# Optimization experiments

Hardware: AMD Instinct MI355X
Metric: run time of the kernel (lower is better)

The kernel has to match this reference:

```python
import jax, jax.numpy as jnp
import numpy as np

V, E, L, D, B, S = 50000, 512, 1024, 10, 1024, 50
N_NODES = L - 1  # internal Huffman nodes (balanced tree from uniform label counts)
LN_EPS = 1e-5
N_HIDDEN = 10


def _build_tree():
    # balanced binary tree in heap order: node at depth t for leaf l is (2^t - 1) + (l >> (D - t))
    l = np.arange(L)[:, None]
    t = np.arange(D)[None, :]
    bits = ((l >> (D - 1 - t)) & 1).astype(np.int32)          # [L, D] path direction bits
    paths = ((2 ** t - 1) + (l >> (D - t))).astype(np.int32)  # [L, D] internal node ids
    return paths, bits


def setup_inputs() -> dict:
    key = jax.random.key(0)
    k1, k2, k3, k4, k5, k6 = jax.random.split(key, 6)
    paths, bits = _build_tree()
    return {
        "input_ids": jax.random.randint(k1, (B, S), 0, V),
        "emb_table": jax.random.normal(k2, (V, E), dtype=jnp.float32) * 0.02,
        "W_h": jax.random.normal(k3, (E, E), dtype=jnp.float32) * (1.0 / np.sqrt(E)),
        "b_h": jax.random.normal(k4, (E,), dtype=jnp.float32) * 0.01,
        "theta_W": jax.random.normal(k5, (N_NODES, E, 2), dtype=jnp.float32) * (1.0 / np.sqrt(E)),
        "theta_b": jax.random.normal(k6, (N_NODES, 2), dtype=jnp.float32) * 0.01,
        "paths": jnp.asarray(paths),
        "bits": jnp.asarray(bits),
    }


def reference(input_ids, emb_table, W_h, b_h, theta_W, theta_b, paths, bits):
    # embedding + mean pool over sequence
    x = jnp.take(emb_table, input_ids, axis=0).mean(axis=1)  # [B, E]
    # LayerNorm with default (non-learned) affine, created fresh in torch forward
    mu = x.mean(axis=-1, keepdims=True)
    var = x.var(axis=-1, keepdims=True)
    x = (x - mu) * jax.lax.rsqrt(var + LN_EPS)
    # repeated hidden linear (same weights, hidden_num times)
    for _ in range(N_HIDDEN):
        x = x @ W_h + b_h
    # hierarchical softmax: batched 2-way logits at every internal node
    logits = jnp.einsum('be,ned->bnd', x, theta_W) + theta_b  # [B, N, 2]
    probs = jax.nn.softmax(logits, axis=-1)                   # [B, N, 2]
    # gather each class's path probs and multiply along the path
    p = probs[:, paths, bits]                                  # [B, L, D]
    return jnp.prod(p, axis=-1)                                # [B, L]
```

## Files before the change

### kernel.cpp

```cpp
#include <hip/hip_runtime.h>
#include <hip/hip_bf16.h>
#include <math.h>

#define B_  1024
#define S_  50
#define E_  512
#define L_  1024
#define D_  10
#define NN  1023
#define LN_EPS 1e-5f
#define CBLK 72

typedef short short8 __attribute__((ext_vector_type(8)));
typedef float f32x4  __attribute__((ext_vector_type(4)));
typedef unsigned short u16;
typedef unsigned int   u32;

union PackU { unsigned int u[4]; short8 s; };

__device__ inline void split8(const float r[8], short8& hi, short8& lo) {
    PackU H, L;
#pragma unroll
    for (int q = 0; q < 4; ++q) {
        const unsigned int u0 = __float_as_uint(r[2*q+0]);
        const unsigned int u1 = __float_as_uint(r[2*q+1]);
        H.u[q] = (u0 >> 16) | (u1 & 0xFFFF0000u);
        const float h0 = __uint_as_float(u0 & 0xFFFF0000u);
        const float h1 = __uint_as_float(u1 & 0xFFFF0000u);
        const float l0 = r[2*q+0] - h0;
        const float l1 = r[2*q+1] - h1;
        unsigned int p;
        asm("v_cvt_pk_bf16_f32 %0, %1, %2" : "=v"(p) : "v"(l0), "v"(l1));
        L.u[q] = p;
    }
    hi = H.s; lo = L.s;
}

__device__ inline void split1(float v, u16& h, u16& l) {
    const unsigned int u = __float_as_uint(v);
    h = (u16)(u >> 16);
    const float hf = __uint_as_float(u & 0xFFFF0000u);
    const float lo = v - hf;
    unsigned int p;
    asm("v_cvt_pk_bf16_f32 %0, %1, %2" : "=v"(p) : "v"(lo), "v"(lo));
    l = (u16)(p & 0xFFFFu);
}

__device__ inline void split2(float v0, float v1, u32& hw, u32& lw) {
    const unsigned int u0 = __float_as_uint(v0);
    const unsigned int u1 = __float_as_uint(v1);
    hw = (u0 >> 16) | (u1 & 0xFFFF0000u);
    const float h0 = __uint_as_float(u0 & 0xFFFF0000u);
    const float h1 = __uint_as_float(u1 & 0xFFFF0000u);
    const float l0 = v0 - h0;
    const float l1 = v1 - h1;
    asm("v_cvt_pk_bf16_f32 %0, %1, %2" : "=v"(lw) : "v"(l0), "v"(l1));
}

struct BFrag { short8 ah[2], al[2], bh[2], bl[2]; };

__device__ inline void loadB(BFrag& f,
                             const u16* pah0, const u16* pal0,
                             const u16* pah1, const u16* pal1,
                             const u16* pbh0, const u16* pbl0,
                             const u16* pbh1, const u16* pbl1, int off) {
    f.ah[0] = *reinterpret_cast<const short8*>(pah0 + off);
    f.al[0] = *reinterpret_cast<const short8*>(pal0 + off);
    f.ah[1] = *reinterpret_cast<const short8*>(pah1 + off);
    f.al[1] = *reinterpret_cast<const short8*>(pal1 + off);
    f.bh[0] = *reinterpret_cast<const short8*>(pbh0 + off);
    f.bl[0] = *reinterpret_cast<const short8*>(pbl0 + off);
    f.bh[1] = *reinterpret_cast<const short8*>(pbh1 + off);
    f.bl[1] = *reinterpret_cast<const short8*>(pbl1 + off);
}

template<int TERMS>
__device__ inline void compB(const BFrag& f, f32x4 acc[2][2]) {
#pragma unroll
    for (int i = 0; i < 2; ++i)
#pragma unroll
        for (int j = 0; j < 2; ++j) {
            acc[i][j] = __builtin_amdgcn_mfma_f32_16x16x32_bf16(f.ah[i], f.bh[j], acc[i][j], 0, 0, 0);
            acc[i][j] = __builtin_amdgcn_mfma_f32_16x16x32_bf16(f.ah[i], f.bl[j], acc[i][j], 0, 0, 0);
            acc[i][j] = __builtin_amdgcn_mfma_f32_16x16x32_bf16(f.al[i], f.bh[j], acc[i][j], 0, 0, 0);
            if (TERMS == 4)
                acc[i][j] = __builtin_amdgcn_mfma_f32_16x16x32_bf16(f.al[i], f.bl[j], acc[i][j], 0, 0, 0);
        }
}

template<int TERMS>
__device__ inline void gemmB(const u16* pah0, const u16* pal0,
                             const u16* pah1, const u16* pal1,
                             const u16* pbh0, const u16* pbl0,
                             const u16* pbh1, const u16* pbl1,
                             f32x4 acc[2][2]) {
    BFrag f0, f1;
    loadB(f0, pah0, pal0, pah1, pal1, pbh0, pbl0, pbh1, pbl1, 0);
#pragma unroll 1
    for (int kt = 0; kt < 16; kt += 2) {
        loadB(f1, pah0, pal0, pah1, pal1, pbh0, pbl0, pbh1, pbl1, (kt + 1) * 32);
        compB<TERMS>(f0, acc);
        if (kt + 2 < 16) loadB(f0, pah0, pal0, pah1, pal1, pbh0, pbl0, pbh1, pbl1, (kt + 2) * 32);
        compB<TERMS>(f1, acc);
    }
}

__device__ inline void do_embed_row(const int* __restrict__ ids,
                                    const float* __restrict__ emb,
                                    u16* __restrict__ xah, u16* __restrict__ xal, int b) {
    const int t = threadIdx.x;
    float a0 = 0.f, a1 = 0.f;
    const int* idr = ids + b * S_;
#pragma unroll 5
    for (int s = 0; s < S_; ++s) {
        const float2 v = *reinterpret_cast<const float2*>(emb + (long)idr[s] * E_ + 2 * t);
        a0 += v.x;
        a1 += v.y;
    }
    a0 *= (1.f / S_);
    a1 *= (1.f / S_);

    __shared__ float red[256];
    red[t] = a0 + a1;
    __syncthreads();
    for (int off = 128; off > 0; off >>= 1) {
        if (t < off) red[t] += red[t + off];
        __syncthreads();
    }
    const float mean = red[0] * (1.f / E_);
    __syncthreads();
    const float d0 = a0 - mean, d1 = a1 - mean;
    red[t] = d0 * d0 + d1 * d1;
    __syncthreads();
    for (int off = 128; off > 0; off >>= 1) {
        if (t < off) red[t] += red[t + off];
        __syncthreads();
    }
    const float var = red[0] * (1.f / E_);
    const float inv = 1.f / sqrtf(var + LN_EPS);
    u32 hw, lw;
    split2(d0 * inv, d1 * inv, hw, lw);
    *reinterpret_cast<u32*>(xah + (long)b * E_ + 2 * t) = hw;
    *reinterpret_cast<u32*>(xal + (long)b * E_ + 2 * t) = lw;
}

__device__ inline void do_dpack(const float* __restrict__ thW,
                                u16* __restrict__ Dh, u16* __restrict__ Dl, int part) {
    const int total = NN * 256;
    const int nth = 64 * 256;
    for (int p = part * 256 + (int)threadIdx.x; p < total; p += nth) {
        const int n = p >> 8;
        const int kp = p & 255;
        const float4 v = *reinterpret_cast<const float4*>(thW + (long)n * 1024 + kp * 4);
        u32 hw, lw;
        split2(v.y - v.x, v.w - v.z, hw, lw);
        *reinterpret_cast<u32*>(Dh + (long)n * E_ + kp * 2) = hw;
        *reinterpret_cast<u32*>(Dl + (long)n * E_ + kp * 2) = lw;
    }
}

__device__ inline void compose_epilogue(f32x4 acc[2][2], int row_base, int col_base,
                                        int kg, int r_lo,
                                        const float* __restrict__ Bbias,
                                        u16* __restrict__ Ch, u16* __restrict__ Cl,
                                        u16* __restrict__ Th, u16* __restrict__ Tl,
                                        float* __restrict__ cvec) {
#pragma unroll
    for (int j = 0; j < 2; ++j) {
        const int col = col_base + j * 16 + r_lo;
        const float bb = Bbias[col];
#pragma unroll
        for (int i = 0; i < 2; ++i) {
            const int row0 = row_base + i * 16 + kg * 4;
            union { ushort4 v; u16 e[4]; } th, tl;
#pragma unroll
            for (int r2 = 0; r2 < 4; ++r2) {
                const int row = row0 + r2;
                float v = acc[i][j][r2];
                if (row == E_) { v += bb; cvec[col] = v; }
                u16 h, l;
                split1(v, h, l);
                if (row <= E_ && Ch != nullptr) {
                    Ch[(long)row * E_ + col] = h;
                    Cl[(long)row * E_ + col] = l;
                }
                th.e[r2] = h; tl.e[r2] = l;
            }
            if (row0 + 3 < E_) {
                *reinterpret_cast<ushort4*>(Th + (long)col * E_ + row0) = th.v;
                *reinterpret_cast<ushort4*>(Tl + (long)col * E_ + row0) = tl.v;
            }
        }
    }
}

__device__ inline void do_compose0(const float* __restrict__ Wh, const float* __restrict__ bh,
                                   u16* __restrict__ Ch, u16* __restrict__ Cl,
                                   u16* __restrict__ Th, u16* __restrict__ Tl,
                                   float* __restrict__ cvec, int bid) {
    const int tid  = threadIdx.x;
    const int wid  = tid >> 6;
    const int lane = tid & 63;
    const int r_lo = lane & 15;
    const int kg   = lane >> 4;
    const int row_base = (bid >> 3) * 64 + (wid >> 1) * 32;
    const int col_base = (bid & 7) * 64 + (wid & 1) * 32;
    f32x4 acc[2][2] = {};
#pragma unroll 2
    for (int kt = 0; kt < E_; kt += 32) {
        const int ks = kt + kg * 8;
        short8 ah[2], al[2], bhf[2], blf[2];
#pragma unroll
        for (int i = 0; i < 2; ++i) {
            const int row = row_base + i * 16 + r_lo;
            const float* ap = (row < E_) ? (Wh + (long)row * E_ + ks) : (bh + ks);
            const float4 v0 = *reinterpret_cast<const float4*>(ap);
            const float4 v1 = *reinterpret_cast<const float4*>(ap + 4);
            const float rr[8] = {v0.x, v0.y, v0.z, v0.w, v1.x, v1.y, v1.z, v1.w};
            split8(rr, ah[i], al[i]);
        }
#pragma unroll
        for (int j = 0; j < 2; ++j) {
            const int c = col_base + j * 16 + r_lo;
            float rr[8];
#pragma unroll
            for (int q = 0; q < 8; ++q) rr[q] = Wh[(long)(ks + q) * E_ + c];
            split8(rr, bhf[j], blf[j]);
        }
#pragma unroll
        for (int i = 0; i < 2; ++i)
#pragma unroll
            for (int j = 0; j < 2; ++j) {
                acc[i][j] = __builtin_amdgcn_mfma_f32_16x16x32_bf16(ah[i], bhf[j], acc[i][j], 0, 0, 0);
                acc[i][j] = __builtin_amdgcn_mfma_f32_16x16x32_bf16(ah[i], blf[j], acc[i][j], 0, 0, 0);
                acc[i][j] = __builtin_amdgcn_mfma_f32_16x16x32_bf16(al[i], bhf[j], acc[i][j], 0, 0, 0);
                acc[i][j] = __builtin_amdgcn_mfma_f32_16x16x32_bf16(al[i], blf[j], acc[i][j], 0, 0, 0);
            }
    }
    compose_epilogue(acc, row_base, col_base, kg, r_lo, bh, Ch, Cl, Th, Tl, cvec);
}

__device__ inline void do_composeB(const u16* __restrict__ Ah, const u16* __restrict__ Al,
                                   const u16* __restrict__ Bh, const u16* __restrict__ Bl,
                                   const float* __restrict__ Bbias,
                                   u16* __restrict__ Ch, u16* __restrict__ Cl,
                                   u16* __restrict__ Th, u16* __restrict__ Tl,
                                   float* __restrict__ cvec, int bid) {
    const int tid  = threadIdx.x;
    const int wid  = tid >> 6;
    const int lane = tid & 63;
    const int r_lo = lane & 15;
    const int kg   = lane >> 4;
    const int row_base = (bid >> 3) * 64 + (wid >> 1) * 32;
    const int col_base = (bid & 7) * 64 + (wid & 1) * 32;

    int ra0 = row_base + r_lo;        if (ra0 > E_) ra0 = E_;
    int ra1 = row_base + 16 + r_lo;   if (ra1 > E_) ra1 = E_;
    const long rb0 = col_base + r_lo;
    const long rb1 = col_base + 16 + r_lo;

    f32x4 acc[2][2] = {};
    gemmB<4>(Ah + (long)ra0 * E_ + kg * 8, Al + (long)ra0 * E_ + kg * 8,
             Ah + (long)ra1 * E_ + kg * 8, Al + (long)ra1 * E_ + kg * 8,
             Bh + rb0 * E_ + kg * 8,       Bl + rb0 * E_ + kg * 8,
             Bh + rb1 * E_ + kg * 8,       Bl + rb1 * E_ + kg * 8, acc);

    compose_epilogue(acc, row_base, col_base, kg, r_lo, Bbias, Ch, Cl, Th, Tl, cvec);
}

__device__ inline void do_applyB(const u16* __restrict__ Xh, const u16* __restrict__ Xl,
                                 const u16* __restrict__ Mh, const u16* __restrict__ Ml,
                                 const float* __restrict__ cvec,
                                 u16* __restrict__ Yh, u16* __restrict__ Yl,
                                 int tr, int tc) {
    const int tid  = threadIdx.x;
    const int wid  = tid >> 6;
    const int lane = tid & 63;
    const int r_lo = lane & 15;
    const int kg   = lane >> 4;
    const int row_base = tr * 64 + (wid >> 1) * 32;
    const int col_base = tc * 64 + (wid & 1) * 32;

    const long ra0 = row_base + r_lo;
    const long ra1 = row_base + 16 + r_lo;
    const long rb0 = col_base + r_lo;
    const long rb1 = col_base + 16 + r_lo;

    f32x4 acc[2][2] = {};
    gemmB<3>(Xh + ra0 * E_ + kg * 8, Xl + ra0 * E_ + kg * 8,
             Xh + ra1 * E_ + kg * 8, Xl + ra1 * E_ + kg * 8,
             Mh + rb0 * E_ + kg * 8, Ml + rb0 * E_ + kg * 8,
             Mh + rb1 * E_ + kg * 8, Ml + rb1 * E_ + kg * 8, acc);

#pragma unroll
    for (int j = 0; j < 2; ++j) {
        const int col = col_base + j * 16 + r_lo;
        const float bb = cvec[col];
#pragma unroll
        for (int i = 0; i < 2; ++i) {
#pragma unroll
            for (int r2 = 0; r2 < 4; ++r2) {
                const int row = row_base + i * 16 + kg * 4 + r2;
                u16 h, l;
                split1(acc[i][j][r2] + bb, h, l);
                Yh[(long)row * E_ + col] = h;
                Yl[(long)row * E_ + col] = l;
            }
        }
    }
}

__global__ __launch_bounds__(256) void k_fused0(const float* __restrict__ Wh,
                                                const float* __restrict__ bh,
                                                u16* __restrict__ Ch0, u16* __restrict__ Cl0,
                                                u16* __restrict__ Th0, u16* __restrict__ Tl0,
                                                float* __restrict__ cvec0,
                                                const int* __restrict__ ids,
                                                const float* __restrict__ emb,
                                                u16* __restrict__ xah, u16* __restrict__ xal,
                                                const float* __restrict__ thW,
                                                u16* __restrict__ Dh, u16* __restrict__ Dl) {
    const int bid = blockIdx.x;
    if (bid < CBLK)            do_compose0(Wh, bh, Ch0, Cl0, Th0, Tl0, cvec0, bid);
    else if (bid < CBLK + 512) do_embed_row(ids, emb, xah, xal, bid - CBLK);
    else                       do_dpack(thW, Dh, Dl, bid - CBLK - 512);
}

__global__ __launch_bounds__(256) void k_fused1(const u16* __restrict__ Ch0, const u16* __restrict__ Cl0,
                                                const u16* __restrict__ Th0, const u16* __restrict__ Tl0,
                                                const float* __restrict__ cvec0,
                                                u16* __restrict__ Ch1, u16* __restrict__ Cl1,
                                                u16* __restrict__ Th1, u16* __restrict__ Tl1,
                                                float* __restrict__ cvec1,
                                                const int* __restrict__ ids,
                                                const float* __restrict__ emb,
                                                u16* __restrict__ xah, u16* __restrict__ xal) {
    const int bid = blockIdx.x;
    if (bid < CBLK) do_composeB(Ch0, Cl0, Th0, Tl0, cvec0, Ch1, Cl1, Th1, Tl1, cvec1, bid);
    else            do_embed_row(ids, emb, xah, xal, 512 + (bid - CBLK));
}

__global__ __launch_bounds__(256) void k_fused2(const u16* __restrict__ Ch1, const u16* __restrict__ Cl1,
                                                const u16* __restrict__ Th1, const u16* __restrict__ Tl1,
                                                const float* __restrict__ cvec1,
                                                u16* __restrict__ Th2, u16* __restrict__ Tl2,
                                                float* __restrict__ cvec2,
                                                const u16* __restrict__ xah, const u16* __restrict__ xal,
                                                const u16* __restrict__ Th0, const u16* __restrict__ Tl0,
                                                const float* __restrict__ cvec0,
                                                u16* __restrict__ y1h, u16* __restrict__ y1l) {
    const int bid = blockIdx.x;
    if (bid < CBLK) {
        do_composeB(Ch1, Cl1, Th1, Tl1, cvec1, nullptr, nullptr, Th2, Tl2, cvec2, bid);
    } else {
        const int t = bid - CBLK;
        do_applyB(xah, xal, Th0, Tl0, cvec0, y1h, y1l, t >> 3, t & 7);
    }
}

__global__ __launch_bounds__(256) void k_apply8(const u16* __restrict__ y1h, const u16* __restrict__ y1l,
                                                const u16* __restrict__ Th2, const u16* __restrict__ Tl2,
                                                const float* __restrict__ cvec2,
                                                u16* __restrict__ y2h, u16* __restrict__ y2l) {
    do_applyB(y1h, y1l, Th2, Tl2, cvec2, y2h, y2l, blockIdx.x >> 3, blockIdx.x & 7);
}

__global__ __launch_bounds__(256) void k_theta(const u16* __restrict__ Xh, const u16* __restrict__ Xl,
                                               const u16* __restrict__ Dh, const u16* __restrict__ Dl,
                                               const float* __restrict__ thb,
                                               float* __restrict__ Sm) {
    const int tid  = threadIdx.x;
    const int wid  = tid >> 6;
    const int lane = tid & 63;
    const int r_lo = lane & 15;
    const int kg   = lane >> 4;
    const int tr = blockIdx.x >> 4;
    const int tc = blockIdx.x & 15;
    const int row_base = tr * 64 + (wid >> 1) * 32;
    const int col_base = tc * 64 + (wid & 1) * 32;

    long c0 = col_base + r_lo;        if (c0 > NN - 1) c0 = NN - 1;
    long c1 = col_base + 16 + r_lo;   if (c1 > NN - 1) c1 = NN - 1;
    const long ra0 = row_base + r_lo;
    const long ra1 = row_base + 16 + r_lo;

    f32x4 acc[2][2] = {};
    gemmB<3>(Xh + ra0 * E_ + kg * 8, Xl + ra0 * E_ + kg * 8,
             Xh + ra1 * E_ + kg * 8, Xl + ra1 * E_ + kg * 8,
             Dh + c0 * E_ + kg * 8,  Dl + c0 * E_ + kg * 8,
             Dh + c1 * E_ + kg * 8,  Dl + c1 * E_ + kg * 8, acc);

#pragma unroll
    for (int j = 0; j < 2; ++j) {
        const int col = col_base + j * 16 + r_lo;
        const int cc = (col > NN - 1) ? (NN - 1) : col;
        const float bb = thb[2 * cc + 1] - thb[2 * cc + 0];
#pragma unroll
        for (int i = 0; i < 2; ++i) {
#pragma unroll
            for (int r2 = 0; r2 < 4; ++r2) {
                const int row = row_base + i * 16 + kg * 4 + r2;
                if (col < NN) {
                    Sm[(long)row * NN + col] = acc[i][j][r2] + bb;
                }
            }
        }
    }
}

__global__ __launch_bounds__(256) void k_leaf_tree(const float* __restrict__ Sm,
                                                   float* __restrict__ out) {
    __shared__ float buf[2][L_];
    const int b = blockIdx.x;
    const int tid = threadIdx.x;
    const float* srow = Sm + (long)b * NN;
    if (tid == 0) buf[0][0] = 1.f;
    __syncthreads();
    int cur = 0;
    for (int t = 0; t < D_; ++t) {
        const int cnt = 1 << t;
        const int base = cnt - 1;
        for (int j = tid; j < cnt; j += 256) {
            const float z = srow[base + j];
            const float s = 1.f / (1.f + __expf(-z));
            const float a = buf[cur][j];
            buf[cur ^ 1][2*j + 1] = a * s;
            buf[cur ^ 1][2*j + 0] = a - a * s;
        }
        __syncthreads();
        cur ^= 1;
    }
    reinterpret_cast<float4*>(out + (long)b * L_)[tid] =
        reinterpret_cast<const float4*>(buf[cur])[tid];
}

extern "C" void kernel_launch(void* const* d_in, const int* in_sizes, int n_in,
                              void* d_out, int out_size, void* d_ws, size_t ws_size,
                              hipStream_t stream) {
    const int*   ids = (const int*)d_in[0];
    const float* emb = (const float*)d_in[1];
    const float* Wh  = (const float*)d_in[2];
    const float* bh  = (const float*)d_in[3];
    const float* thW = (const float*)d_in[4];
    const float* thb = (const float*)d_in[5];
    float* out = (float*)d_out;

    char* ws = (char*)d_ws;
    const size_t MB = 1u << 20;
    u16* xah = (u16*)(ws + 0 * MB);
    u16* xal = (u16*)(ws + 1 * MB);
    u16* y1h = (u16*)(ws + 2 * MB);
    u16* y1l = (u16*)(ws + 3 * MB);
    u16* y2h = (u16*)(ws + 4 * MB);
    u16* y2l = (u16*)(ws + 5 * MB);
    float* sm = (float*)(ws + 6 * MB);
    u16* Dh  = (u16*)(ws + 11 * MB);
    u16* Dl  = (u16*)(ws + 12 * MB);
    u16* Ch0 = (u16*)(ws + 13 * MB);
    u16* Cl0 = (u16*)(ws + 14 * MB);
    u16* Ch1 = (u16*)(ws + 15 * MB);
    u16* Cl1 = (u16*)(ws + 16 * MB);
    u16* Th0 = (u16*)(ws + 17 * MB);
    u16* Tl0 = (u16*)(ws + 17 * MB + 512 * 1024);
    u16* Th1 = (u16*)(ws + 18 * MB);
    u16* Tl1 = (u16*)(ws + 18 * MB + 512 * 1024);
    u16* Th2 = (u16*)(ws + 19 * MB);
    u16* Tl2 = (u16*)(ws + 19 * MB + 512 * 1024);
    float* cvec0 = (float*)(ws + 20 * MB);
    float* cvec1 = (float*)(ws + 20 * MB + 4096);
    float* cvec2 = (float*)(ws + 20 * MB + 8192);

    k_fused0<<<CBLK + 512 + 64, 256, 0, stream>>>(Wh, bh, Ch0, Cl0, Th0, Tl0, cvec0,
                                                  ids, emb, xah, xal, thW, Dh, Dl);

    k_fused1<<<CBLK + 512, 256, 0, stream>>>(Ch0, Cl0, Th0, Tl0, cvec0,
                                             Ch1, Cl1, Th1, Tl1, cvec1,
                                             ids, emb, xah, xal);

    k_fused2<<<CBLK + 128, 256, 0, stream>>>(Ch1, Cl1, Th1, Tl1, cvec1,
                                             Th2, Tl2, cvec2,
                                             xah, xal, Th0, Tl0, cvec0, y1h, y1l);

    k_apply8<<<128, 256, 0, stream>>>(y1h, y1l, Th2, Tl2, cvec2, y2h, y2l);

    k_theta<<<256, 256, 0, stream>>>(y2h, y2l, Dh, Dl, thb, sm);

    k_leaf_tree<<<B_, 256, 0, stream>>>(sm, out);
}
```

Measured before the change: 105.2 us.

## Fuse final apply, theta GEMM and leaf-tree product into one kernel

Replaces the last three kernels (final hidden apply, theta logits GEMM, per-row tree product) with a single kernel. Each 16-row block keeps its hidden activations and sigmoids in shared memory and computes leaf probabilities directly from the path bits. This removes two launches and the global round trips through y2 and the 1024x1023 logit matrix. In exchange it runs only 64 blocks, which is low occupancy on a large GPU, and each block re-reads the full Th2 and D weight matrices.

```diff
diff --git a/kernel.cpp b/kernel.cpp
--- a/kernel.cpp
+++ b/kernel.cpp
@@ -102,6 +102,90 @@
         compB<TERMS>(f0, acc);
         if (kt + 2 < 16) loadB(f0, pah0, pal0, pah1, pal1, pbh0, pbl0, pbh1, pbl1, (kt + 2) * 32);
         compB<TERMS>(f1, acc);
+    }
+}
+
+struct F12 { short8 ah, al, bh0, bl0, bh1, bl1; };
+
+__device__ inline void ld12(F12& f, const u16* pah, const u16* pal,
+                            const u16* pbh0, const u16* pbl0,
+                            const u16* pbh1, const u16* pbl1, int off) {
+    f.ah  = *reinterpret_cast<const short8*>(pah + off);
+    f.al  = *reinterpret_cast<const short8*>(pal + off);
+    f.bh0 = *reinterpret_cast<const short8*>(pbh0 + off);
+    f.bl0 = *reinterpret_cast<const short8*>(pbl0 + off);
+    f.bh1 = *reinterpret_cast<const short8*>(pbh1 + off);
+    f.bl1 = *reinterpret_cast<const short8*>(pbl1 + off);
+}
+
+__device__ inline void cp12(const F12& f, f32x4 acc[2]) {
+    acc[0] = __builtin_amdgcn_mfma_f32_16x16x32_bf16(f.ah, f.bh0, acc[0], 0, 0, 0);
+    acc[0] = __builtin_amdgcn_mfma_f32_16x16x32_bf16(f.ah, f.bl0, acc[0], 0, 0, 0);
+    acc[0] = __builtin_amdgcn_mfma_f32_16x16x32_bf16(f.al, f.bh0, acc[0], 0, 0, 0);
+    acc[1] = __builtin_amdgcn_mfma_f32_16x16x32_bf16(f.ah, f.bh1, acc[1], 0, 0, 0);
+    acc[1] = __builtin_amdgcn_mfma_f32_16x16x32_bf16(f.ah, f.bl1, acc[1], 0, 0, 0);
+    acc[1] = __builtin_amdgcn_mfma_f32_16x16x32_bf16(f.al, f.bh1, acc[1], 0, 0, 0);
+}
+
+__device__ inline void gemm1x2(const u16* pah, const u16* pal,
+                               const u16* pbh0, const u16* pbl0,
+                               const u16* pbh1, const u16* pbl1,
+                               f32x4 acc[2]) {
+    F12 f0, f1;
+    ld12(f0, pah, pal, pbh0, pbl0, pbh1, pbl1, 0);
+#pragma unroll 1
+    for (int kt = 0; kt < 16; kt += 2) {
+        ld12(f1, pah, pal, pbh0, pbl0, pbh1, pbl1, (kt + 1) * 32);
+        cp12(f0, acc);
+        if (kt + 2 < 16) ld12(f0, pah, pal, pbh0, pbl0, pbh1, pbl1, (kt + 2) * 32);
+        cp12(f1, acc);
+    }
+}
+
+struct B12 { short8 bh0, bl0, bh1, bl1; };
+
+__device__ inline void ldB12(B12& g, const u16* pbh0, const u16* pbl0,
+                             const u16* pbh1, const u16* pbl1, int off) {
+    g.bh0 = *reinterpret_cast<const short8*>(pbh0 + off);
+    g.bl0 = *reinterpret_cast<const short8*>(pbl0 + off);
+    g.bh1 = *reinterpret_cast<const short8*>(pbh1 + off);
+    g.bl1 = *reinterpret_cast<const short8*>(pbl1 + off);
+}
+
+__device__ inline void ldA_lds(const float* y2f, int r_lo, int kg, int kt,
+                               short8& ah, short8& al) {
+    const int k0 = kg * 8 + kt * 32;
+    const int idx = (r_lo * 512 + k0) ^ ((r_lo & 7) << 3);
+    const float4 a0 = *reinterpret_cast<const float4*>(&y2f[idx]);
+    const float4 a1 = *reinterpret_cast<const float4*>(&y2f[idx + 4]);
+    const float rr[8] = {a0.x, a0.y, a0.z, a0.w, a1.x, a1.y, a1.z, a1.w};
+    split8(rr, ah, al);
+}
+
+__device__ inline void cpA12(const short8& ah, const short8& al, const B12& g, f32x4 acc[2]) {
+    acc[0] = __builtin_amdgcn_mfma_f32_16x16x32_bf16(ah, g.bh0, acc[0], 0, 0, 0);
+    acc[0] = __builtin_amdgcn_mfma_f32_16x16x32_bf16(ah, g.bl0, acc[0], 0, 0, 0);
+    acc[0] = __builtin_amdgcn_mfma_f32_16x16x32_bf16(al, g.bh0, acc[0], 0, 0, 0);
+    acc[1] = __builtin_amdgcn_mfma_f32_16x16x32_bf16(ah, g.bh1, acc[1], 0, 0, 0);
+    acc[1] = __builtin_amdgcn_mfma_f32_16x16x32_bf16(ah, g.bl1, acc[1], 0, 0, 0);
+    acc[1] = __builtin_amdgcn_mfma_f32_16x16x32_bf16(al, g.bh1, acc[1], 0, 0, 0);
+}
+
+__device__ inline void gemm1x2_ldsA(const float* y2f, int r_lo, int kg,
+                                    const u16* pbh0, const u16* pbl0,
+                                    const u16* pbh1, const u16* pbl1,
+                                    f32x4 acc[2]) {
+    B12 g0, g1;
+    ldB12(g0, pbh0, pbl0, pbh1, pbl1, 0);
+#pragma unroll 1
+    for (int kt = 0; kt < 16; kt += 2) {
+        ldB12(g1, pbh0, pbl0, pbh1, pbl1, (kt + 1) * 32);
+        short8 ah, al;
+        ldA_lds(y2f, r_lo, kg, kt, ah, al);
+        cpA12(ah, al, g0, acc);
+        if (kt + 2 < 16) ldB12(g0, pbh0, pbl0, pbh1, pbl1, (kt + 2) * 32);
+        ldA_lds(y2f, r_lo, kg, kt + 1, ah, al);
+        cpA12(ah, al, g1, acc);
     }
 }
 
@@ -358,80 +442,94 @@
     }
 }
 
-__global__ __launch_bounds__(256) void k_apply8(const u16* __restrict__ y1h, const u16* __restrict__ y1l,
-                                                const u16* __restrict__ Th2, const u16* __restrict__ Tl2,
-                                                const float* __restrict__ cvec2,
-                                                u16* __restrict__ y2h, u16* __restrict__ y2l) {
-    do_applyB(y1h, y1l, Th2, Tl2, cvec2, y2h, y2l, blockIdx.x >> 3, blockIdx.x & 7);
-}
-
-__global__ __launch_bounds__(256) void k_theta(const u16* __restrict__ Xh, const u16* __restrict__ Xl,
+__global__ __launch_bounds__(256) void k_final(const u16* __restrict__ y1h, const u16* __restrict__ y1l,
+                                               const u16* __restrict__ Th2, const u16* __restrict__ Tl2,
+                                               const float* __restrict__ cvec2,
                                                const u16* __restrict__ Dh, const u16* __restrict__ Dl,
                                                const float* __restrict__ thb,
-                                               float* __restrict__ Sm) {
+                                               float* __restrict__ out) {
+    __shared__ float y2f[16 * 512];
+    __shared__ float sig[16][1024];
     const int tid  = threadIdx.x;
     const int wid  = tid >> 6;
     const int lane = tid & 63;
     const int r_lo = lane & 15;
     const int kg   = lane >> 4;
-    const int tr = blockIdx.x >> 4;
-    const int tc = blockIdx.x & 15;
-    const int row_base = tr * 64 + (wid >> 1) * 32;
-    const int col_base = tc * 64 + (wid & 1) * 32;
-
-    long c0 = col_base + r_lo;        if (c0 > NN - 1) c0 = NN - 1;
-    long c1 = col_base + 16 + r_lo;   if (c1 > NN - 1) c1 = NN - 1;
-    const long ra0 = row_base + r_lo;
-    const long ra1 = row_base + 16 + r_lo;
-
-    f32x4 acc[2][2] = {};
-    gemmB<3>(Xh + ra0 * E_ + kg * 8, Xl + ra0 * E_ + kg * 8,
-             Xh + ra1 * E_ + kg * 8, Xl + ra1 * E_ + kg * 8,
-             Dh + c0 * E_ + kg * 8,  Dl + c0 * E_ + kg * 8,
-             Dh + c1 * E_ + kg * 8,  Dl + c1 * E_ + kg * 8, acc);
-
-#pragma unroll
-    for (int j = 0; j < 2; ++j) {
-        const int col = col_base + j * 16 + r_lo;
-        const int cc = (col > NN - 1) ? (NN - 1) : col;
-        const float bb = thb[2 * cc + 1] - thb[2 * cc + 0];
-#pragma unroll
-        for (int i = 0; i < 2; ++i) {
-#pragma unroll
-            for (int r2 = 0; r2 < 4; ++r2) {
-                const int row = row_base + i * 16 + kg * 4 + r2;
-                if (col < NN) {
-                    Sm[(long)row * NN + col] = acc[i][j][r2] + bb;
+    const int r0   = blockIdx.x * 16;
+
+    {
+        const long arow = r0 + r_lo;
+        const u16* pah = y1h + arow * E_ + kg * 8;
+        const u16* pal = y1l + arow * E_ + kg * 8;
+#pragma unroll 1
+        for (int pair = 0; pair < 4; ++pair) {
+            const int c0 = wid * 128 + pair * 32 + r_lo;
+            const int c1 = c0 + 16;
+            f32x4 acc[2] = {};
+            gemm1x2(pah, pal,
+                    Th2 + (long)c0 * E_ + kg * 8, Tl2 + (long)c0 * E_ + kg * 8,
+                    Th2 + (long)c1 * E_ + kg * 8, Tl2 + (long)c1 * E_ + kg * 8, acc);
+#pragma unroll
+            for (int j = 0; j < 2; ++j) {
+                const int col = (j == 0) ? c0 : c1;
+                const float bb = cvec2[col];
+#pragma unroll
+                for (int r2 = 0; r2 < 4; ++r2) {
+                    const int row = kg * 4 + r2;
+                    y2f[(row * 512 + col) ^ ((row & 7) << 3)] = acc[j][r2] + bb;
                 }
             }
         }
     }
-}
-
-__global__ __launch_bounds__(256) void k_leaf_tree(const float* __restrict__ Sm,
-                                                   float* __restrict__ out) {
-    __shared__ float buf[2][L_];
-    const int b = blockIdx.x;
-    const int tid = threadIdx.x;
-    const float* srow = Sm + (long)b * NN;
-    if (tid == 0) buf[0][0] = 1.f;
     __syncthreads();
-    int cur = 0;
-    for (int t = 0; t < D_; ++t) {
-        const int cnt = 1 << t;
-        const int base = cnt - 1;
-        for (int j = tid; j < cnt; j += 256) {
-            const float z = srow[base + j];
-            const float s = 1.f / (1.f + __expf(-z));
-            const float a = buf[cur][j];
-            buf[cur ^ 1][2*j + 1] = a * s;
-            buf[cur ^ 1][2*j + 0] = a - a * s;
-        }
-        __syncthreads();
-        cur ^= 1;
-    }
-    reinterpret_cast<float4*>(out + (long)b * L_)[tid] =
-        reinterpret_cast<const float4*>(buf[cur])[tid];
+
+    {
+#pragma unroll 1
+        for (int pair = 0; pair < 8; ++pair) {
+            const int c0 = wid * 256 + pair * 32 + r_lo;
+            const int c1 = c0 + 16;
+            const long cc0 = (c0 > NN - 1) ? (NN - 1) : c0;
+            const long cc1 = (c1 > NN - 1) ? (NN - 1) : c1;
+            f32x4 acc[2] = {};
+            gemm1x2_ldsA(y2f, r_lo, kg,
+                         Dh + cc0 * E_ + kg * 8, Dl + cc0 * E_ + kg * 8,
+                         Dh + cc1 * E_ + kg * 8, Dl + cc1 * E_ + kg * 8, acc);
+#pragma unroll
+            for (int j = 0; j < 2; ++j) {
+                const int col = (j == 0) ? c0 : c1;
+                const long cc = (j == 0) ? cc0 : cc1;
+                const float g = thb[2 * cc + 1] - thb[2 * cc];
+#pragma unroll
+                for (int r2 = 0; r2 < 4; ++r2) {
+                    const int row = kg * 4 + r2;
+                    const float z = acc[j][r2] + g;
+                    sig[row][col] = 1.f / (1.f + __expf(-z));
+                }
+            }
+        }
+    }
+    __syncthreads();
+
+    {
+#pragma unroll 1
+        for (int rr = 0; rr < 4; ++rr) {
+            const int row = wid * 4 + rr;
+            float* orow = out + (long)(r0 + row) * L_;
+#pragma unroll 1
+            for (int i = 0; i < 16; ++i) {
+                const int l = i * 64 + lane;
+                float p = 1.f;
+#pragma unroll
+                for (int t = 0; t < D_; ++t) {
+                    const int node = (1 << t) - 1 + (l >> (D_ - t));
+                    const int bit  = (l >> (D_ - 1 - t)) & 1;
+                    const float s = sig[row][node];
+                    p *= bit ? s : (1.f - s);
+                }
+                orow[l] = p;
+            }
+        }
+    }
 }
 
 extern "C" void kernel_launch(void* const* d_in, const int* in_sizes, int n_in,
@@ -451,9 +549,6 @@
     u16* xal = (u16*)(ws + 1 * MB);
     u16* y1h = (u16*)(ws + 2 * MB);
     u16* y1l = (u16*)(ws + 3 * MB);
-    u16* y2h = (u16*)(ws + 4 * MB);
-    u16* y2l = (u16*)(ws + 5 * MB);
-    float* sm = (float*)(ws + 6 * MB);
     u16* Dh  = (u16*)(ws + 11 * MB);
     u16* Dl  = (u16*)(ws + 12 * MB);
     u16* Ch0 = (u16*)(ws + 13 * MB);
@@ -481,9 +576,5 @@
                                              Th2, Tl2, cvec2,
                                              xah, xal, Th0, Tl0, cvec0, y1h, y1l);
 
-    k_apply8<<<128, 256, 0, stream>>>(y1h, y1l, Th2, Tl2, cvec2, y2h, y2l);
-
-    k_theta<<<256, 256, 0, stream>>>(y2h, y2l, Dh, Dl, thb, sm);
-
-    k_leaf_tree<<<B_, 256, 0, stream>>>(sm, out);
-}
+    k_final<<<64, 256, 0, stream>>>(y1h, y1l, Th2, Tl2, cvec2, Dh, Dl, thb, out);
+}
```

Result: slower. 177.6 us (+68.9%).

## Restructure hidden-layer chain schedule, fuse sigmoid into theta GEMM, gather leaf paths

Applied to the files above, without the earlier changes.

Embedding of all 1024 rows now runs in the first fused launch, which removes one compose level (W^2 to W^4 only). The hidden stack is then applied through three apply passes instead of two, with a change in how the powers of W are split between them. The sigmoid moves into the theta GEMM epilogue, which writes a padded 1024-wide probability row. The leaf kernel becomes a per-leaf gather-product over the 10 path nodes instead of a level-by-level tree expansion with a barrier per level. This trades one fewer compose step for an extra dependent apply launch.

```diff
diff --git a/kernel.cpp b/kernel.cpp
--- a/kernel.cpp
+++ b/kernel.cpp
@@ -321,54 +321,38 @@
                                                 const float* __restrict__ thW,
                                                 u16* __restrict__ Dh, u16* __restrict__ Dl) {
     const int bid = blockIdx.x;
-    if (bid < CBLK)            do_compose0(Wh, bh, Ch0, Cl0, Th0, Tl0, cvec0, bid);
-    else if (bid < CBLK + 512) do_embed_row(ids, emb, xah, xal, bid - CBLK);
-    else                       do_dpack(thW, Dh, Dl, bid - CBLK - 512);
+    if (bid < CBLK)             do_compose0(Wh, bh, Ch0, Cl0, Th0, Tl0, cvec0, bid);
+    else if (bid < CBLK + 1024) do_embed_row(ids, emb, xah, xal, bid - CBLK);
+    else                        do_dpack(thW, Dh, Dl, bid - CBLK - 1024);
 }
 
 __global__ __launch_bounds__(256) void k_fused1(const u16* __restrict__ Ch0, const u16* __restrict__ Cl0,
                                                 const u16* __restrict__ Th0, const u16* __restrict__ Tl0,
                                                 const float* __restrict__ cvec0,
-                                                u16* __restrict__ Ch1, u16* __restrict__ Cl1,
                                                 u16* __restrict__ Th1, u16* __restrict__ Tl1,
                                                 float* __restrict__ cvec1,
-                                                const int* __restrict__ ids,
-                                                const float* __restrict__ emb,
-                                                u16* __restrict__ xah, u16* __restrict__ xal) {
-    const int bid = blockIdx.x;
-    if (bid < CBLK) do_composeB(Ch0, Cl0, Th0, Tl0, cvec0, Ch1, Cl1, Th1, Tl1, cvec1, bid);
-    else            do_embed_row(ids, emb, xah, xal, 512 + (bid - CBLK));
-}
-
-__global__ __launch_bounds__(256) void k_fused2(const u16* __restrict__ Ch1, const u16* __restrict__ Cl1,
-                                                const u16* __restrict__ Th1, const u16* __restrict__ Tl1,
-                                                const float* __restrict__ cvec1,
-                                                u16* __restrict__ Th2, u16* __restrict__ Tl2,
-                                                float* __restrict__ cvec2,
                                                 const u16* __restrict__ xah, const u16* __restrict__ xal,
-                                                const u16* __restrict__ Th0, const u16* __restrict__ Tl0,
-                                                const float* __restrict__ cvec0,
                                                 u16* __restrict__ y1h, u16* __restrict__ y1l) {
     const int bid = blockIdx.x;
     if (bid < CBLK) {
-        do_composeB(Ch1, Cl1, Th1, Tl1, cvec1, nullptr, nullptr, Th2, Tl2, cvec2, bid);
+        do_composeB(Ch0, Cl0, Th0, Tl0, cvec0, nullptr, nullptr, Th1, Tl1, cvec1, bid);
     } else {
         const int t = bid - CBLK;
         do_applyB(xah, xal, Th0, Tl0, cvec0, y1h, y1l, t >> 3, t & 7);
     }
 }
 
-__global__ __launch_bounds__(256) void k_apply8(const u16* __restrict__ y1h, const u16* __restrict__ y1l,
-                                                const u16* __restrict__ Th2, const u16* __restrict__ Tl2,
-                                                const float* __restrict__ cvec2,
-                                                u16* __restrict__ y2h, u16* __restrict__ y2l) {
-    do_applyB(y1h, y1l, Th2, Tl2, cvec2, y2h, y2l, blockIdx.x >> 3, blockIdx.x & 7);
-}
-
-__global__ __launch_bounds__(256) void k_theta(const u16* __restrict__ Xh, const u16* __restrict__ Xl,
-                                               const u16* __restrict__ Dh, const u16* __restrict__ Dl,
-                                               const float* __restrict__ thb,
-                                               float* __restrict__ Sm) {
+__global__ __launch_bounds__(256) void k_apply(const u16* __restrict__ Yh, const u16* __restrict__ Yl,
+                                               const u16* __restrict__ Th1, const u16* __restrict__ Tl1,
+                                               const float* __restrict__ cvec1,
+                                               u16* __restrict__ Zh, u16* __restrict__ Zl) {
+    do_applyB(Yh, Yl, Th1, Tl1, cvec1, Zh, Zl, blockIdx.x >> 3, blockIdx.x & 7);
+}
+
+__global__ __launch_bounds__(256) void k_theta_sig(const u16* __restrict__ Xh, const u16* __restrict__ Xl,
+                                                   const u16* __restrict__ Dh, const u16* __restrict__ Dl,
+                                                   const float* __restrict__ thb,
+                                                   float* __restrict__ sig) {
     const int tid  = threadIdx.x;
     const int wid  = tid >> 6;
     const int lane = tid & 63;
@@ -394,44 +378,43 @@
     for (int j = 0; j < 2; ++j) {
         const int col = col_base + j * 16 + r_lo;
         const int cc = (col > NN - 1) ? (NN - 1) : col;
-        const float bb = thb[2 * cc + 1] - thb[2 * cc + 0];
+        const float g = thb[2 * cc + 1] - thb[2 * cc + 0];
 #pragma unroll
         for (int i = 0; i < 2; ++i) {
 #pragma unroll
             for (int r2 = 0; r2 < 4; ++r2) {
                 const int row = row_base + i * 16 + kg * 4 + r2;
                 if (col < NN) {
-                    Sm[(long)row * NN + col] = acc[i][j][r2] + bb;
+                    const float z = acc[i][j][r2] + g;
+                    sig[(long)row * 1024 + col] = 1.f / (1.f + __expf(-z));
                 }
             }
         }
     }
 }
 
-__global__ __launch_bounds__(256) void k_leaf_tree(const float* __restrict__ Sm,
-                                                   float* __restrict__ out) {
-    __shared__ float buf[2][L_];
+__global__ __launch_bounds__(256) void k_leaf_gather(const float* __restrict__ sig,
+                                                     float* __restrict__ out) {
+    __shared__ float s[1024];
     const int b = blockIdx.x;
     const int tid = threadIdx.x;
-    const float* srow = Sm + (long)b * NN;
-    if (tid == 0) buf[0][0] = 1.f;
+    reinterpret_cast<float4*>(s)[tid] =
+        reinterpret_cast<const float4*>(sig + (long)b * 1024)[tid];
     __syncthreads();
-    int cur = 0;
-    for (int t = 0; t < D_; ++t) {
-        const int cnt = 1 << t;
-        const int base = cnt - 1;
-        for (int j = tid; j < cnt; j += 256) {
-            const float z = srow[base + j];
-            const float s = 1.f / (1.f + __expf(-z));
-            const float a = buf[cur][j];
-            buf[cur ^ 1][2*j + 1] = a * s;
-            buf[cur ^ 1][2*j + 0] = a - a * s;
-        }
-        __syncthreads();
-        cur ^= 1;
-    }
-    reinterpret_cast<float4*>(out + (long)b * L_)[tid] =
-        reinterpret_cast<const float4*>(buf[cur])[tid];
+    float* orow = out + (long)b * L_;
+#pragma unroll 1
+    for (int q = 0; q < 4; ++q) {
+        const int l = q * 256 + tid;
+        float p = 1.f;
+#pragma unroll
+        for (int t = 0; t < D_; ++t) {
+            const int node = (1 << t) - 1 + (l >> (D_ - t));
+            const int bit  = (l >> (D_ - 1 - t)) & 1;
+            const float sv = s[node];
+            p *= bit ? sv : (1.f - sv);
+        }
+        orow[l] = p;
+    }
 }
 
 extern "C" void kernel_launch(void* const* d_in, const int* in_sizes, int n_in,
@@ -453,37 +436,32 @@
     u16* y1l = (u16*)(ws + 3 * MB);
     u16* y2h = (u16*)(ws + 4 * MB);
     u16* y2l = (u16*)(ws + 5 * MB);
-    float* sm = (float*)(ws + 6 * MB);
-    u16* Dh  = (u16*)(ws + 11 * MB);
-    u16* Dl  = (u16*)(ws + 12 * MB);
-    u16* Ch0 = (u16*)(ws + 13 * MB);
-    u16* Cl0 = (u16*)(ws + 14 * MB);
-    u16* Ch1 = (u16*)(ws + 15 * MB);
-    u16* Cl1 = (u16*)(ws + 16 * MB);
-    u16* Th0 = (u16*)(ws + 17 * MB);
-    u16* Tl0 = (u16*)(ws + 17 * MB + 512 * 1024);
-    u16* Th1 = (u16*)(ws + 18 * MB);
-    u16* Tl1 = (u16*)(ws + 18 * MB + 512 * 1024);
-    u16* Th2 = (u16*)(ws + 19 * MB);
-    u16* Tl2 = (u16*)(ws + 19 * MB + 512 * 1024);
-    float* cvec0 = (float*)(ws + 20 * MB);
-    float* cvec1 = (float*)(ws + 20 * MB + 4096);
-    float* cvec2 = (float*)(ws + 20 * MB + 8192);
-
-    k_fused0<<<CBLK + 512 + 64, 256, 0, stream>>>(Wh, bh, Ch0, Cl0, Th0, Tl0, cvec0,
-                                                  ids, emb, xah, xal, thW, Dh, Dl);
-
-    k_fused1<<<CBLK + 512, 256, 0, stream>>>(Ch0, Cl0, Th0, Tl0, cvec0,
-                                             Ch1, Cl1, Th1, Tl1, cvec1,
-                                             ids, emb, xah, xal);
-
-    k_fused2<<<CBLK + 128, 256, 0, stream>>>(Ch1, Cl1, Th1, Tl1, cvec1,
-                                             Th2, Tl2, cvec2,
-                                             xah, xal, Th0, Tl0, cvec0, y1h, y1l);
-
-    k_apply8<<<128, 256, 0, stream>>>(y1h, y1l, Th2, Tl2, cvec2, y2h, y2l);
-
-    k_theta<<<256, 256, 0, stream>>>(y2h, y2l, Dh, Dl, thb, sm);
-
-    k_leaf_tree<<<B_, 256, 0, stream>>>(sm, out);
-}
+    u16* y3h = (u16*)(ws + 6 * MB);
+    u16* y3l = (u16*)(ws + 7 * MB);
+    float* sig = (float*)(ws + 8 * MB);
+    u16* Dh  = (u16*)(ws + 12 * MB);
+    u16* Dl  = (u16*)(ws + 13 * MB);
+    u16* Ch0 = (u16*)(ws + 14 * MB);
+    u16* Cl0 = (u16*)(ws + 15 * MB);
+    u16* Th0 = (u16*)(ws + 16 * MB);
+    u16* Tl0 = (u16*)(ws + 16 * MB + 512 * 1024);
+    u16* Th1 = (u16*)(ws + 17 * MB);
+    u16* Tl1 = (u16*)(ws + 17 * MB + 512 * 1024);
+    float* cvec0 = (float*)(ws + 18 * MB);
+    float* cvec1 = (float*)(ws + 18 * MB + 4096);
+
+    k_fused0<<<CBLK + 1024 + 64, 256, 0, stream>>>(Wh, bh, Ch0, Cl0, Th0, Tl0, cvec0,
+                                                   ids, emb, xah, xal, thW, Dh, Dl);
+
+    k_fused1<<<CBLK + 128, 256, 0, stream>>>(Ch0, Cl0, Th0, Tl0, cvec0,
+                                             Th1, Tl1, cvec1,
+                                             xah, xal, y1h, y1l);
+
+    k_apply<<<128, 256, 0, stream>>>(y1h, y1l, Th1, Tl1, cvec1, y2h, y2l);
+
+    k_apply<<<128, 256, 0, stream>>>(y2h, y2l, Th1, Tl1, cvec1, y3h, y3l);
+
+    k_theta_sig<<<256, 256, 0, stream>>>(y3h, y3l, Dh, Dl, thb, sig);
+
+    k_leaf_gather<<<B_, 256, 0, stream>>>(sig, out);
+}
```

After: 100.5 us. 1.05x faster.
